# Optimization experiments

Hardware: AMD Instinct MI355X
Metric: run time of the kernel (lower is better)

The kernel has to match this reference:

```python
import jax, jax.numpy as jnp
import numpy as np

D_MODEL = 1024
N_HEADS = 16
HEAD_DIM = D_MODEL // N_HEADS
B, S = 4, 2048


def setup_inputs() -> dict:
    key = jax.random.key(0)
    ks = jax.random.split(key, 12)
    s = 1.0 / np.sqrt(D_MODEL)
    inp = {
        'query': jax.random.normal(ks[0], (B, S, D_MODEL), jnp.float32),
        'key': jax.random.normal(ks[1], (B, S, D_MODEL), jnp.float32),
        'value': jax.random.normal(ks[2], (B, S, D_MODEL), jnp.float32),
        # causal mask, broadcast over batch and heads: [1,1,S,S]
        'mask': jnp.tril(jnp.ones((S, S), jnp.int32))[None, None],
        'Wq': jax.random.normal(ks[3], (D_MODEL, D_MODEL), jnp.float32) * s,
        'bq': jnp.zeros((D_MODEL,), jnp.float32),
        'Wk': jax.random.normal(ks[4], (D_MODEL, D_MODEL), jnp.float32) * s,
        'bk': jnp.zeros((D_MODEL,), jnp.float32),
        'Wv': jax.random.normal(ks[5], (D_MODEL, D_MODEL), jnp.float32) * s,
        'bv': jnp.zeros((D_MODEL,), jnp.float32),
        'Wo': jax.random.normal(ks[6], (D_MODEL, D_MODEL), jnp.float32) * s,
        'bo': jnp.zeros((D_MODEL,), jnp.float32),
    }
    return inp


def reference(query, key, value, mask, Wq, bq, Wk, bk, Wv, bv, Wo, bo):
    b, q_len, _ = query.shape
    scale = jnp.sqrt(jnp.float32(HEAD_DIM))
    # projections
    q = query @ Wq + bq
    k = key @ Wk + bk
    v = value @ Wv + bv
    # [b, h, s, hd]
    q = q.reshape(b, q_len, N_HEADS, HEAD_DIM).transpose(0, 2, 1, 3)
    k = k.reshape(b, -1, N_HEADS, HEAD_DIM).transpose(0, 2, 1, 3)
    v = v.reshape(b, -1, N_HEADS, HEAD_DIM).transpose(0, 2, 1, 3)
    scores = jnp.einsum('bhqd,bhkd->bhqk', q, k) / scale
    scores = jnp.where(mask == 0, jnp.float32(-jnp.inf), scores)
    attn = jax.nn.softmax(scores, axis=-1)  # dropout p=0 / eval mode
    out = jnp.einsum('bhqk,bhkd->bhqd', attn, v)
    out = out.transpose(0, 2, 1, 3).reshape(b, q_len, D_MODEL)
    return out @ Wo + bo
```

## Files before the change

### kernel.cpp

```cpp
#include <hip/hip_runtime.h>
#include <hip/hip_bf16.h>

typedef __attribute__((ext_vector_type(8))) short short8;
typedef __attribute__((ext_vector_type(4))) float floatx4;
typedef __attribute__((ext_vector_type(4))) unsigned short ushort4v;

#define D_MODEL 1024
#define S_LEN   2048
#define N_HEADS 16
#define HEAD_DIM 64
#define BATCH   4

__device__ __forceinline__ unsigned short f2bf(float x) {
    union { float f; unsigned int u; } v; v.f = x;
    unsigned int u = v.u;
    unsigned int r = (u + 0x7FFFu + ((u >> 16) & 1u)) >> 16;
    return (unsigned short)r;
}
__device__ __forceinline__ unsigned short f2bf_trunc(float x) {
    union { float f; unsigned int u; } v; v.f = x;
    return (unsigned short)(v.u >> 16);
}

__device__ __forceinline__ void gload_lds16(const void* g, void* s) {
    __builtin_amdgcn_global_load_lds(
        (const __attribute__((address_space(1))) void*)g,
        (__attribute__((address_space(3))) void*)s, 16, 0, 0);
}

struct Conv3 {
    const float* src[3];
    unsigned short* dst[3];
};

__global__ __launch_bounds__(256) void conv_bf16(Conv3 a) {
    const float* s = a.src[blockIdx.z];
    unsigned short* d = a.dst[blockIdx.z];
    size_t i = ((size_t)blockIdx.x * 256 + threadIdx.x) * 8;
    float4 f0 = *(const float4*)(s + i);
    float4 f1 = *(const float4*)(s + i + 4);
    short8 v;
    v[0] = (short)f2bf(f0.x); v[1] = (short)f2bf(f0.y);
    v[2] = (short)f2bf(f0.z); v[3] = (short)f2bf(f0.w);
    v[4] = (short)f2bf(f1.x); v[5] = (short)f2bf(f1.y);
    v[6] = (short)f2bf(f1.z); v[7] = (short)f2bf(f1.w);
    *(short8*)(d + i) = v;
}

struct Trans4 {
    const float* W[4];
    unsigned short* Wt[4];
};

__global__ __launch_bounds__(256) void transpose_w(Trans4 args) {
    __shared__ unsigned short tile[32][33];
    const float* W = args.W[blockIdx.z];
    unsigned short* Wt = args.Wt[blockIdx.z];
    int n0 = blockIdx.x * 32;
    int k0 = blockIdx.y * 32;
    int t = threadIdx.x;
    int r = t >> 5, c = t & 31;
    for (int i = 0; i < 4; ++i) {
        int k = k0 + r + i * 8;
        tile[r + i * 8][c] = f2bf(W[(size_t)k * D_MODEL + n0 + c]);
    }
    __syncthreads();
    for (int i = 0; i < 4; ++i) {
        int n = n0 + r + i * 8;
        Wt[(size_t)n * D_MODEL + k0 + c] = tile[c][r + i * 8];
    }
}

struct GemmIn {
    const unsigned short* A;
    const unsigned short* Bt;
    const float* bias;
    void* C;
    int mode;
};
struct Gemm3 { GemmIn g[3]; };

#define BAR()   asm volatile("s_barrier" ::: "memory")
#define LGKM0() asm volatile("s_waitcnt lgkmcnt(0)" ::: "memory")
#define VMW4()  asm volatile("s_waitcnt vmcnt(4)" ::: "memory")
#define VMW0()  asm volatile("s_waitcnt vmcnt(0)" ::: "memory")

#define READ_A(BUF, H)                                                         \
    _Pragma("unroll") for (int ii = 0; ii < 4; ++ii) {                         \
        aF[ii][0] = *(const short8*)&lds[(BUF)*32768 + aOff + ((H)*4+ii)*512]; \
        aF[ii][1] = *(const short8*)&lds[(BUF)*32768 + aOff + ((H)*4+ii)*512 + 4096]; \
    }
#define READ_B(BUF, J0, DST)                                                   \
    _Pragma("unroll") for (int jj = 0; jj < 2; ++jj) {                         \
        DST[jj][0] = *(const short8*)&lds[(BUF)*32768 + bOff + ((J0)+jj)*512]; \
        DST[jj][1] = *(const short8*)&lds[(BUF)*32768 + bOff + ((J0)+jj)*512 + 4096]; \
    }
#define MFMA_Q(I0, BREG, J0)                                                   \
    __builtin_amdgcn_s_setprio(1);                                             \
    _Pragma("unroll") for (int ii = 0; ii < 4; ++ii)                           \
    _Pragma("unroll") for (int jj = 0; jj < 2; ++jj) {                         \
        acc[(I0)+ii][(J0)+jj] = __builtin_amdgcn_mfma_f32_16x16x32_bf16(       \
            aF[ii][0], BREG[jj][0], acc[(I0)+ii][(J0)+jj], 0, 0, 0);           \
        acc[(I0)+ii][(J0)+jj] = __builtin_amdgcn_mfma_f32_16x16x32_bf16(       \
            aF[ii][1], BREG[jj][1], acc[(I0)+ii][(J0)+jj], 0, 0, 0);           \
    }                                                                          \
    __builtin_amdgcn_s_setprio(0)

__global__ __launch_bounds__(512, 2) void gemm_256(Gemm3 args) {
    constexpr int K = D_MODEL, N = D_MODEL;
    constexpr int NT = K / 64;
    constexpr int NI = NT / 2;
    GemmIn g = args.g[blockIdx.z];

    __shared__ __align__(16) unsigned short lds[65536];

    const int m0 = blockIdx.x * 256;
    const int n0 = blockIdx.y * 256;
    const int t = threadIdx.x;
    const int w = t >> 6, lane = t & 63;
    const int quad = lane >> 4, l16 = lane & 15;
    const int wm = w >> 2, wn = w & 3;

    const int srow = w * 16 + (lane >> 2);
    const int scol = ((lane & 3) * 8) ^ ((lane & 32) ? 16 : 0);

    const int fx = (quad * 8) ^ ((l16 & 8) ? 16 : 0);
    const int aOff = wm * 8192 + l16 * 32 + fx;
    const int bOff = 16384 + (wn >> 1) * 8192 + ((wn & 1) * 64 + l16) * 32 + fx;

    floatx4 acc[8][4] = {};
    short8 aF[4][2], bLo[2][2], bHi[2][2];

    auto stageA = [&](int buf, int h, int kt) {
        const unsigned short* src =
            g.A + (size_t)(m0 + h * 128 + srow) * K + kt * 64 + scol;
        unsigned short* dst = &lds[buf * 32768 + h * 8192 + w * 512];
        gload_lds16(src, dst);
        gload_lds16(src + 32, dst + 4096);
    };
    auto stageB = [&](int buf, int h, int kt) {
        const unsigned short* src =
            g.Bt + (size_t)(n0 + h * 128 + srow) * K + kt * 64 + scol;
        unsigned short* dst = &lds[buf * 32768 + 16384 + h * 8192 + w * 512];
        gload_lds16(src, dst);
        gload_lds16(src + 32, dst + 4096);
    };

    stageB(0, 0, 0); stageB(0, 1, 0);
    stageA(0, 0, 0); stageA(0, 1, 0);
    stageB(1, 0, 1); stageB(1, 1, 1);
    VMW4();
    BAR();

    for (int n = 0; n < NI - 1; ++n) {
        const int t0 = 2 * n;
        READ_A(0, 0); READ_B(0, 0, bLo);
        stageA(1, 0, t0 + 1);
        BAR(); LGKM0();
        MFMA_Q(0, bLo, 0);
        BAR();
        READ_B(0, 2, bHi);
        stageA(1, 1, t0 + 1);
        BAR(); LGKM0();
        MFMA_Q(0, bHi, 2);
        BAR();
        READ_A(0, 1);
        stageB(0, 0, t0 + 2);
        BAR(); LGKM0();
        MFMA_Q(4, bHi, 2);
        BAR();
        stageB(0, 1, t0 + 2);
        VMW4();
        BAR();
        MFMA_Q(4, bLo, 0);
        BAR();
        READ_A(1, 0); READ_B(1, 0, bLo);
        stageA(0, 0, t0 + 2);
        BAR(); LGKM0();
        MFMA_Q(0, bLo, 0);
        BAR();
        READ_B(1, 2, bHi);
        stageA(0, 1, t0 + 2);
        BAR(); LGKM0();
        MFMA_Q(0, bHi, 2);
        BAR();
        READ_A(1, 1);
        stageB(1, 0, t0 + 3);
        BAR(); LGKM0();
        MFMA_Q(4, bHi, 2);
        BAR();
        stageB(1, 1, t0 + 3);
        VMW4();
        BAR();
        MFMA_Q(4, bLo, 0);
        BAR();
    }

    {
        READ_A(0, 0); READ_B(0, 0, bLo);
        stageA(1, 0, NT - 1);
        BAR(); LGKM0();
        MFMA_Q(0, bLo, 0);
        BAR();
        READ_B(0, 2, bHi);
        stageA(1, 1, NT - 1);
        BAR(); LGKM0();
        MFMA_Q(0, bHi, 2);
        BAR();
        READ_A(0, 1);
        BAR(); LGKM0();
        MFMA_Q(4, bHi, 2);
        BAR();
        VMW0();
        BAR();
        MFMA_Q(4, bLo, 0);
        BAR();
        READ_A(1, 0); READ_B(1, 0, bLo);
        BAR(); LGKM0();
        MFMA_Q(0, bLo, 0);
        BAR();
        READ_B(1, 2, bHi);
        BAR(); LGKM0();
        MFMA_Q(0, bHi, 2);
        BAR();
        READ_A(1, 1);
        BAR(); LGKM0();
        MFMA_Q(4, bHi, 2);
        BAR();
        BAR();
        MFMA_Q(4, bLo, 0);
        BAR();
    }

    if (g.mode == 2) {
        unsigned short* Ct = (unsigned short*)g.C;
#pragma unroll
        for (int j = 0; j < 4; ++j) {
            int col = n0 + wn * 64 + j * 16 + l16;
            int h = col >> 6, dd = col & 63;
            float bv = g.bias[col];
#pragma unroll
            for (int i = 0; i < 8; ++i) {
                int row0 = m0 + wm * 128 + i * 16 + quad * 4;
                int bb = row0 >> 11, s = row0 & 2047;
                ushort4v u;
#pragma unroll
                for (int r = 0; r < 4; ++r) u[r] = f2bf(acc[i][j][r] + bv);
                *(ushort4v*)(Ct + ((size_t)(bb * 16 + h) * 64 + dd) * 2048 + s) = u;
            }
        }
    } else {
#pragma unroll
        for (int j = 0; j < 4; ++j) {
            int col = n0 + wn * 64 + j * 16 + l16;
            float bv = g.bias[col];
#pragma unroll
            for (int i = 0; i < 8; ++i) {
#pragma unroll
                for (int r = 0; r < 4; ++r) {
                    int row = m0 + wm * 128 + i * 16 + quad * 4 + r;
                    float v = acc[i][j][r] + bv;
                    if (g.mode == 1)
                        ((float*)g.C)[(size_t)row * N + col] = v;
                    else
                        ((unsigned short*)g.C)[(size_t)row * N + col] = f2bf(v);
                }
            }
        }
    }
}

__global__ __launch_bounds__(512) void flash_attn(
    const unsigned short* __restrict__ Qp,
    const unsigned short* __restrict__ Kp,
    const unsigned short* __restrict__ Vtg,
    unsigned short* __restrict__ Op) {
    constexpr int S = S_LEN, D = D_MODEL;
    __shared__ __align__(16) unsigned short Ks[64 * 64];
    __shared__ __align__(16) unsigned short Vs[64 * 64];
    __shared__ __align__(16) unsigned short Ps[8][16][72];

    int pair = blockIdx.x;
    int bh = blockIdx.y;
    int b = bh >> 4;
    int t = threadIdx.x;
    int wave = t >> 6, lane = t & 63;
    int quad = lane >> 4, l16 = lane & 15;

    const size_t head_off = (size_t)b * S * D + (size_t)(bh & 15) * HEAD_DIM;
    const unsigned short* Khead = Kp + head_off;
    const unsigned short* Vhead = Vtg + (size_t)bh * 64 * S;

    int q0l = pair * 128, q0h = (15 - pair) * 128;
    int qgl = q0l + wave * 16 + l16;
    int qgh = q0h + wave * 16 + l16;

    const unsigned short* qpl = Qp + head_off + (size_t)qgl * D + quad * 8;
    short8 ql0 = *(const short8*)qpl, ql1 = *(const short8*)(qpl + 32);
    const unsigned short* qph = Qp + head_off + (size_t)qgh * D + quad * 8;
    short8 qh0 = *(const short8*)qph, qh1 = *(const short8*)(qph + 32);

    floatx4 ol[4] = {}, oh[4] = {};
    float ll = 0.f, lh = 0.f;
    const float cs = 0.125f * 1.44269504088896340736f;

    int sw = wave & 3;
    bool doK = wave < 4;
    int srow = sw * 16 + (lane >> 2);
    int scol = (lane & 3) * 8;
    unsigned short* sdst0 = (doK ? Ks : Vs) + sw * 512;
    unsigned short* sdst1 = sdst0 + 2048;

    int wqminl = q0l + wave * 16, wqmaxl = wqminl + 15;
    int wqminh = q0h + wave * 16, wqmaxh = wqminh + 15;

    auto half_step = [&](int k0, int qg, int wqmin, float& l_i,
                         floatx4* o, short8 qb0, short8 qb1) {
        floatx4 st[4];
        for (int gk = 0; gk < 4; ++gk) {
            short8 ka0 = *(const short8*)&Ks[(gk * 16 + l16) * 32 + quad * 8];
            short8 ka1 = *(const short8*)&Ks[2048 + (gk * 16 + l16) * 32 + quad * 8];
            floatx4 s = {};
            s = __builtin_amdgcn_mfma_f32_16x16x32_bf16(ka0, qb0, s, 0, 0, 0);
            s = __builtin_amdgcn_mfma_f32_16x16x32_bf16(ka1, qb1, s, 0, 0, 0);
            st[gk] = s;
        }

        float sv[16];
        float rs = 0.f;
        if (k0 + 63 < wqmin) {
            for (int i = 0; i < 16; ++i) {
                sv[i] = __builtin_amdgcn_exp2f(st[i >> 2][i & 3] * cs);
                rs += sv[i];
            }
        } else {
            for (int gk = 0; gk < 4; ++gk)
                for (int r = 0; r < 4; ++r) {
                    int key = k0 + gk * 16 + quad * 4 + r;
                    float p = (key <= qg)
                        ? __builtin_amdgcn_exp2f(st[gk][r] * cs) : 0.f;
                    sv[gk * 4 + r] = p;
                    rs += p;
                }
        }
        rs += __shfl_xor(rs, 16);
        rs += __shfl_xor(rs, 32);
        l_i += rs;

        for (int gk = 0; gk < 4; ++gk) {
            ushort4v u;
            for (int r = 0; r < 4; ++r) u[r] = f2bf_trunc(sv[gk * 4 + r]);
            *(ushort4v*)&Ps[wave][l16][gk * 16 + quad * 4] = u;
        }

        short8 pf0 = *(const short8*)&Ps[wave][l16][quad * 8];
        short8 pf1 = *(const short8*)&Ps[wave][l16][32 + quad * 8];
        for (int jd = 0; jd < 4; ++jd) {
            short8 va0 = *(const short8*)&Vs[(jd * 16 + l16) * 32 + quad * 8];
            short8 va1 = *(const short8*)&Vs[2048 + (jd * 16 + l16) * 32 + quad * 8];
            o[jd] = __builtin_amdgcn_mfma_f32_16x16x32_bf16(va0, pf0, o[jd], 0, 0, 0);
            o[jd] = __builtin_amdgcn_mfma_f32_16x16x32_bf16(va1, pf1, o[jd], 0, 0, 0);
        }
    };

    int n_kt = 2 * (15 - pair) + 2;
    for (int kt = 0; kt < n_kt; ++kt) {
        int k0 = kt * 64;
        if (doK) {
            gload_lds16(Khead + (size_t)(k0 + srow) * D + scol, sdst0);
            gload_lds16(Khead + (size_t)(k0 + srow) * D + 32 + scol, sdst1);
        } else {
            gload_lds16(Vhead + (size_t)srow * S + k0 + scol, sdst0);
            gload_lds16(Vhead + (size_t)srow * S + k0 + 32 + scol, sdst1);
        }
        __syncthreads();

        if (k0 <= wqmaxl) half_step(k0, qgl, wqminl, ll, ol, ql0, ql1);
        if (k0 <= wqmaxh) half_step(k0, qgh, wqminh, lh, oh, qh0, qh1);
        __syncthreads();
    }

    {
        float inv = 1.0f / ll;
        unsigned short* op = Op + head_off + (size_t)qgl * D;
        for (int jd = 0; jd < 4; ++jd) {
            ushort4v u;
            for (int r = 0; r < 4; ++r) u[r] = f2bf(ol[jd][r] * inv);
            *(ushort4v*)(op + jd * 16 + quad * 4) = u;
        }
    }
    {
        float inv = 1.0f / lh;
        unsigned short* op = Op + head_off + (size_t)qgh * D;
        for (int jd = 0; jd < 4; ++jd) {
            ushort4v u;
            for (int r = 0; r < 4; ++r) u[r] = f2bf(oh[jd][r] * inv);
            *(ushort4v*)(op + jd * 16 + quad * 4) = u;
        }
    }
}

extern "C" void kernel_launch(void* const* d_in, const int* in_sizes, int n_in,
                              void* d_out, int out_size, void* d_ws,
                              size_t ws_size, hipStream_t stream) {
    const float* query = (const float*)d_in[0];
    const float* key   = (const float*)d_in[1];
    const float* value = (const float*)d_in[2];
    const float* Wq = (const float*)d_in[4];
    const float* bq = (const float*)d_in[5];
    const float* Wk = (const float*)d_in[6];
    const float* bk = (const float*)d_in[7];
    const float* Wv = (const float*)d_in[8];
    const float* bv = (const float*)d_in[9];
    const float* Wo = (const float*)d_in[10];
    const float* bo = (const float*)d_in[11];
    float* out = (float*)d_out;

    char* ws = (char*)d_ws;
    const size_t WT_SZ = (size_t)D_MODEL * D_MODEL * 2;
    const size_t X_SZ = (size_t)BATCH * S_LEN * D_MODEL * 2;
    unsigned short* wtq = (unsigned short*)(ws);
    unsigned short* wtk = (unsigned short*)(ws + WT_SZ);
    unsigned short* wtv = (unsigned short*)(ws + 2 * WT_SZ);
    unsigned short* wto = (unsigned short*)(ws + 3 * WT_SZ);
    unsigned short* Qbf = (unsigned short*)(ws + 4 * WT_SZ);
    unsigned short* Kbf = (unsigned short*)(ws + 4 * WT_SZ + X_SZ);
    unsigned short* Vbf = (unsigned short*)(ws + 4 * WT_SZ + 2 * X_SZ);
    unsigned short* Qp  = (unsigned short*)(ws + 4 * WT_SZ + 3 * X_SZ);
    unsigned short* Kp  = (unsigned short*)(ws + 4 * WT_SZ + 4 * X_SZ);
    unsigned short* Vtg = (unsigned short*)(ws + 4 * WT_SZ + 5 * X_SZ);
    unsigned short* Ao  = Qbf;

    Trans4 ta;
    ta.W[0] = Wq; ta.W[1] = Wk; ta.W[2] = Wv; ta.W[3] = Wo;
    ta.Wt[0] = wtq; ta.Wt[1] = wtk; ta.Wt[2] = wtv; ta.Wt[3] = wto;
    transpose_w<<<dim3(32, 32, 4), 256, 0, stream>>>(ta);

    Conv3 ca;
    ca.src[0] = query; ca.src[1] = key; ca.src[2] = value;
    ca.dst[0] = Qbf;   ca.dst[1] = Kbf; ca.dst[2] = Vbf;
    conv_bf16<<<dim3(4096, 1, 3), 256, 0, stream>>>(ca);

    Gemm3 gq;
    gq.g[0].A = Qbf; gq.g[0].Bt = wtq; gq.g[0].bias = bq; gq.g[0].C = Qp;  gq.g[0].mode = 0;
    gq.g[1].A = Kbf; gq.g[1].Bt = wtk; gq.g[1].bias = bk; gq.g[1].C = Kp;  gq.g[1].mode = 0;
    gq.g[2].A = Vbf; gq.g[2].Bt = wtv; gq.g[2].bias = bv; gq.g[2].C = Vtg; gq.g[2].mode = 2;
    gemm_256<<<dim3(32, 4, 3), 512, 0, stream>>>(gq);

    flash_attn<<<dim3(8, BATCH * N_HEADS), 512, 0, stream>>>(
        Qp, Kp, Vtg, Ao);

    Gemm3 go;
    go.g[0].A = Ao; go.g[0].Bt = wto; go.g[0].bias = bo; go.g[0].C = out; go.g[0].mode = 1;
    gemm_256<<<dim3(32, 4, 1), 512, 0, stream>>>(go);
}
```

Before: 348.3 us.

## Shrink GEMM tile to 256x128 to double block count and cut LDS

The projection GEMM tile changes from 256x256 to 256x128. The grid doubles in N, LDS drops to 96KB, and each warp's accumulators halve. The pipeline schedule is rewritten around a single B fragment set, with matching changes to the wait counts and epilogue. The output GEMM previously had only 128 blocks on a 256-CU part, so the goal is better CU utilisation. The cost is lower arithmetic intensity and more global reads of A.

```diff
diff --git a/kernel.cpp b/kernel.cpp
--- a/kernel.cpp
+++ b/kernel.cpp
@@ -82,27 +82,27 @@
 
 #define BAR()   asm volatile("s_barrier" ::: "memory")
 #define LGKM0() asm volatile("s_waitcnt lgkmcnt(0)" ::: "memory")
-#define VMW4()  asm volatile("s_waitcnt vmcnt(4)" ::: "memory")
+#define VMW2()  asm volatile("s_waitcnt vmcnt(2)" ::: "memory")
 #define VMW0()  asm volatile("s_waitcnt vmcnt(0)" ::: "memory")
 
-#define READ_A(BUF, H)                                                         \
+#define READ_A(BUF, I0)                                                        \
     _Pragma("unroll") for (int ii = 0; ii < 4; ++ii) {                         \
-        aF[ii][0] = *(const short8*)&lds[(BUF)*32768 + aOff + ((H)*4+ii)*512]; \
-        aF[ii][1] = *(const short8*)&lds[(BUF)*32768 + aOff + ((H)*4+ii)*512 + 4096]; \
-    }
-#define READ_B(BUF, J0, DST)                                                   \
+        aF[ii][0] = *(const short8*)&lds[(BUF)*24576 + aOff + ((I0)+ii)*512];  \
+        aF[ii][1] = *(const short8*)&lds[(BUF)*24576 + aOff + ((I0)+ii)*512 + 4096]; \
+    }
+#define READ_B(BUF)                                                            \
     _Pragma("unroll") for (int jj = 0; jj < 2; ++jj) {                         \
-        DST[jj][0] = *(const short8*)&lds[(BUF)*32768 + bOff + ((J0)+jj)*512]; \
-        DST[jj][1] = *(const short8*)&lds[(BUF)*32768 + bOff + ((J0)+jj)*512 + 4096]; \
-    }
-#define MFMA_Q(I0, BREG, J0)                                                   \
+        bF[jj][0] = *(const short8*)&lds[(BUF)*24576 + bOff + jj*512];         \
+        bF[jj][1] = *(const short8*)&lds[(BUF)*24576 + bOff + jj*512 + 4096];  \
+    }
+#define MFMA_Q(I0)                                                             \
     __builtin_amdgcn_s_setprio(1);                                             \
     _Pragma("unroll") for (int ii = 0; ii < 4; ++ii)                           \
     _Pragma("unroll") for (int jj = 0; jj < 2; ++jj) {                         \
-        acc[(I0)+ii][(J0)+jj] = __builtin_amdgcn_mfma_f32_16x16x32_bf16(       \
-            aF[ii][0], BREG[jj][0], acc[(I0)+ii][(J0)+jj], 0, 0, 0);           \
-        acc[(I0)+ii][(J0)+jj] = __builtin_amdgcn_mfma_f32_16x16x32_bf16(       \
-            aF[ii][1], BREG[jj][1], acc[(I0)+ii][(J0)+jj], 0, 0, 0);           \
+        acc[(I0)+ii][jj] = __builtin_amdgcn_mfma_f32_16x16x32_bf16(            \
+            aF[ii][0], bF[jj][0], acc[(I0)+ii][jj], 0, 0, 0);                  \
+        acc[(I0)+ii][jj] = __builtin_amdgcn_mfma_f32_16x16x32_bf16(            \
+            aF[ii][1], bF[jj][1], acc[(I0)+ii][jj], 0, 0, 0);                  \
     }                                                                          \
     __builtin_amdgcn_s_setprio(0)
 
@@ -112,10 +112,10 @@
     constexpr int NI = NT / 2;
     GemmIn g = args.g[blockIdx.z];
 
-    __shared__ __align__(16) unsigned short lds[65536];
+    __shared__ __align__(16) unsigned short lds[49152];
 
     const int m0 = blockIdx.x * 256;
-    const int n0 = blockIdx.y * 256;
+    const int n0 = blockIdx.y * 128;
     const int t = threadIdx.x;
     const int w = t >> 6, lane = t & 63;
     const int quad = lane >> 4, l16 = lane & 15;
@@ -126,117 +126,82 @@
 
     const int fx = (quad * 8) ^ ((l16 & 8) ? 16 : 0);
     const int aOff = wm * 8192 + l16 * 32 + fx;
-    const int bOff = 16384 + (wn >> 1) * 8192 + ((wn & 1) * 64 + l16) * 32 + fx;
-
-    floatx4 acc[8][4] = {};
-    short8 aF[4][2], bLo[2][2], bHi[2][2];
+    const int bOff = 16384 + (wn * 32 + l16) * 32 + fx;
+
+    floatx4 acc[8][2] = {};
+    short8 aF[4][2], bF[2][2];
 
     auto stageA = [&](int buf, int h, int kt) {
         const unsigned short* src =
             g.A + (size_t)(m0 + h * 128 + srow) * K + kt * 64 + scol;
-        unsigned short* dst = &lds[buf * 32768 + h * 8192 + w * 512];
+        unsigned short* dst = &lds[buf * 24576 + h * 8192 + w * 512];
         gload_lds16(src, dst);
         gload_lds16(src + 32, dst + 4096);
     };
-    auto stageB = [&](int buf, int h, int kt) {
+    auto stageB = [&](int buf, int kt) {
         const unsigned short* src =
-            g.Bt + (size_t)(n0 + h * 128 + srow) * K + kt * 64 + scol;
-        unsigned short* dst = &lds[buf * 32768 + 16384 + h * 8192 + w * 512];
+            g.Bt + (size_t)(n0 + srow) * K + kt * 64 + scol;
+        unsigned short* dst = &lds[buf * 24576 + 16384 + w * 512];
         gload_lds16(src, dst);
         gload_lds16(src + 32, dst + 4096);
     };
 
-    stageB(0, 0, 0); stageB(0, 1, 0);
-    stageA(0, 0, 0); stageA(0, 1, 0);
-    stageB(1, 0, 1); stageB(1, 1, 1);
-    VMW4();
+    stageA(0, 0, 0); stageA(0, 1, 0); stageB(0, 0);
+    stageB(1, 1);
+    VMW2();
     BAR();
 
     for (int n = 0; n < NI - 1; ++n) {
         const int t0 = 2 * n;
-        READ_A(0, 0); READ_B(0, 0, bLo);
-        stageA(1, 0, t0 + 1);
-        BAR(); LGKM0();
-        MFMA_Q(0, bLo, 0);
-        BAR();
-        READ_B(0, 2, bHi);
-        stageA(1, 1, t0 + 1);
-        BAR(); LGKM0();
-        MFMA_Q(0, bHi, 2);
-        BAR();
-        READ_A(0, 1);
-        stageB(0, 0, t0 + 2);
-        BAR(); LGKM0();
-        MFMA_Q(4, bHi, 2);
-        BAR();
-        stageB(0, 1, t0 + 2);
-        VMW4();
-        BAR();
-        MFMA_Q(4, bLo, 0);
-        BAR();
-        READ_A(1, 0); READ_B(1, 0, bLo);
-        stageA(0, 0, t0 + 2);
-        BAR(); LGKM0();
-        MFMA_Q(0, bLo, 0);
-        BAR();
-        READ_B(1, 2, bHi);
-        stageA(0, 1, t0 + 2);
-        BAR(); LGKM0();
-        MFMA_Q(0, bHi, 2);
-        BAR();
-        READ_A(1, 1);
-        stageB(1, 0, t0 + 3);
-        BAR(); LGKM0();
-        MFMA_Q(4, bHi, 2);
-        BAR();
-        stageB(1, 1, t0 + 3);
-        VMW4();
-        BAR();
-        MFMA_Q(4, bLo, 0);
+        READ_A(0, 0); READ_B(0);
+        stageA(1, 0, t0 + 1); stageA(1, 1, t0 + 1);
+        BAR(); LGKM0();
+        MFMA_Q(0);
+        BAR();
+        READ_A(0, 4);
+        stageB(0, t0 + 2);
+        VMW2();
+        BAR(); LGKM0();
+        MFMA_Q(4);
+        BAR();
+        READ_A(1, 0); READ_B(1);
+        stageA(0, 0, t0 + 2); stageA(0, 1, t0 + 2);
+        BAR(); LGKM0();
+        MFMA_Q(0);
+        BAR();
+        READ_A(1, 4);
+        stageB(1, t0 + 3);
+        VMW2();
+        BAR(); LGKM0();
+        MFMA_Q(4);
         BAR();
     }
 
     {
-        READ_A(0, 0); READ_B(0, 0, bLo);
-        stageA(1, 0, NT - 1);
-        BAR(); LGKM0();
-        MFMA_Q(0, bLo, 0);
-        BAR();
-        READ_B(0, 2, bHi);
-        stageA(1, 1, NT - 1);
-        BAR(); LGKM0();
-        MFMA_Q(0, bHi, 2);
-        BAR();
-        READ_A(0, 1);
-        BAR(); LGKM0();
-        MFMA_Q(4, bHi, 2);
-        BAR();
+        READ_A(0, 0); READ_B(0);
+        stageA(1, 0, NT - 1); stageA(1, 1, NT - 1);
+        BAR(); LGKM0();
+        MFMA_Q(0);
+        BAR();
+        READ_A(0, 4);
         VMW0();
-        BAR();
-        MFMA_Q(4, bLo, 0);
-        BAR();
-        READ_A(1, 0); READ_B(1, 0, bLo);
-        BAR(); LGKM0();
-        MFMA_Q(0, bLo, 0);
-        BAR();
-        READ_B(1, 2, bHi);
-        BAR(); LGKM0();
-        MFMA_Q(0, bHi, 2);
-        BAR();
-        READ_A(1, 1);
-        BAR(); LGKM0();
-        MFMA_Q(4, bHi, 2);
-        BAR();
-        BAR();
-        MFMA_Q(4, bLo, 0);
-        BAR();
+        BAR(); LGKM0();
+        MFMA_Q(4);
+        BAR();
+        READ_A(1, 0); READ_B(1);
+        BAR(); LGKM0();
+        MFMA_Q(0);
+        BAR();
+        READ_A(1, 4);
+        LGKM0();
+        MFMA_Q(4);
     }
 
     if (g.mode == 2) {
         unsigned short* Ct = (unsigned short*)g.C;
 #pragma unroll
-        for (int j = 0; j < 4; ++j) {
-            int col = n0 + wn * 64 + j * 16 + l16;
+        for (int j = 0; j < 2; ++j) {
+            int col = n0 + wn * 32 + j * 16 + l16;
             int h = col >> 6, dd = col & 63;
             float bv = g.bias[col];
 #pragma unroll
@@ -251,8 +216,8 @@
         }
     } else {
 #pragma unroll
-        for (int j = 0; j < 4; ++j) {
-            int col = n0 + wn * 64 + j * 16 + l16;
+        for (int j = 0; j < 2; ++j) {
+            int col = n0 + wn * 32 + j * 16 + l16;
             float bv = g.bias[col];
 #pragma unroll
             for (int i = 0; i < 8; ++i) {
@@ -445,12 +410,12 @@
     gq.g[0].A = Qbf; gq.g[0].Bt = wtq; gq.g[0].bias = bq; gq.g[0].C = Qp;  gq.g[0].mode = 0;
     gq.g[1].A = Kbf; gq.g[1].Bt = wtk; gq.g[1].bias = bk; gq.g[1].C = Kp;  gq.g[1].mode = 0;
     gq.g[2].A = Vbf; gq.g[2].Bt = wtv; gq.g[2].bias = bv; gq.g[2].C = Vtg; gq.g[2].mode = 2;
-    gemm_256<<<dim3(32, 4, 3), 512, 0, stream>>>(gq);
+    gemm_256<<<dim3(32, 8, 3), 512, 0, stream>>>(gq);
 
     flash_attn<<<dim3(8, BATCH * N_HEADS), 512, 0, stream>>>(
         Qp, Kp, Vtg, Ao);
 
     Gemm3 go;
     go.g[0].A = Ao; go.g[0].Bt = wto; go.g[0].bias = bo; go.g[0].C = out; go.g[0].mode = 1;
-    gemm_256<<<dim3(32, 4, 1), 512, 0, stream>>>(go);
-}
+    gemm_256<<<dim3(32, 8, 1), 512, 0, stream>>>(go);
+}
```

After: 336.3 us. 3.4% less time.
